# Optimization experiments

Measured on AMD Instinct MI355X. Metric: run time of the kernel, lower is better.

## Reference

```python
import jax, jax.numpy as jnp
import numpy as np

N = 255  # 17 * time_input(15) graph nodes


def spmm(rows, cols, vals, x):
    """Batched sparse (COO) @ dense: x is [B, N, F] -> [B, N, F]."""
    g = x[:, cols, :] * vals[None, :, None]                      # [B, nnz, F]
    out = jax.ops.segment_sum(jnp.swapaxes(g, 0, 1), rows,
                              num_segments=N)                     # [N, B, F]
    return jnp.swapaxes(out, 0, 1)


def setup_inputs() -> dict:
    key = jax.random.key(0)
    ks = jax.random.split(key, 32)
    B, nnz = 256, 2040
    inp = {"H": jax.random.normal(ks[0], (B, N, 2), jnp.float32)}
    for i, nm in enumerate(["sm_s", "sm_t", "sp_s", "sp_t"]):
        inp[nm + "_rows"] = jax.random.randint(ks[1 + 3 * i], (nnz,), 0, N, jnp.int32)
        inp[nm + "_cols"] = jax.random.randint(ks[2 + 3 * i], (nnz,), 0, N, jnp.int32)
        inp[nm + "_vals"] = jax.random.uniform(ks[3 + 3 * i], (nnz,), jnp.float32)
    dims = [(2, 400), (400, 300), (300, 100), (100, 300), (300, 400), (400, 2)]
    wnames = ["W0", "W1", "W2", "Wd0", "Wd1", "Wd2"]
    for j, (di, do) in enumerate(dims):
        inp[wnames[j]] = jax.random.normal(ks[13 + j], (di, do), jnp.float32) / np.sqrt(di).astype(np.float32)
        inp["b" + wnames[j][1:]] = jnp.zeros((do,), jnp.float32)
    return inp


def reference(H, sm_s_rows, sm_s_cols, sm_s_vals,
              sm_t_rows, sm_t_cols, sm_t_vals,
              sp_s_rows, sp_s_cols, sp_s_vals,
              sp_t_rows, sp_t_cols, sp_t_vals,
              W0, b0, W1, b1, W2, b2, Wd0, bd0, Wd1, bd1, Wd2, bd2):
    def layer(x, W, b, r, c, v):
        # Dense projection fused with Laplacian SpMM + ReLU (same math as the
        # per-sample Python loop in the original, batched over B).
        return jax.nn.relu(spmm(r, c, v, x @ W + b))

    # encoder: Laplacian smoothing (enc0, enc1 with s_DADsm; enc2 with t_DADsm)
    H = layer(H, W0, b0, sm_s_rows, sm_s_cols, sm_s_vals)
    H = layer(H, W1, b1, sm_s_rows, sm_s_cols, sm_s_vals)
    H = layer(H, W2, b2, sm_t_rows, sm_t_cols, sm_t_vals)
    # decoder: Laplacian sharpening (dec0 with t_DADsp; dec1, dec2 with s_DADsp)
    H = layer(H, Wd0, bd0, sp_t_rows, sp_t_cols, sp_t_vals)
    H = layer(H, Wd1, bd1, sp_s_rows, sp_s_cols, sp_s_vals)
    H = layer(H, Wd2, bd2, sp_s_rows, sp_s_cols, sp_s_vals)
    return H  # [B, 255, 2]
```

## Files before the change

### kernel.cpp

```cpp
#include <hip/hip_runtime.h>
#include <hip/hip_bf16.h>


#define NN 255
#define YCH 4096

typedef __attribute__((ext_vector_type(8))) short short8;
typedef __attribute__((ext_vector_type(4))) float floatx4;

__device__ __forceinline__ float bf2f(ushort u) {
    union { uint u; float f; } c; c.u = ((uint)u) << 16; return c.f;
}
__device__ __forceinline__ ushort f2bf(float f) {
    union { float f; uint u; } c; c.f = f;
    uint u = c.u + 0x7fff + ((c.u >> 16) & 1);
    return (ushort)(u >> 16);
}
__device__ __forceinline__ short8 u4_frag(uint4 v) {
    union { uint4 u; short8 s; } c; c.u = v; return c.s;
}
__device__ __forceinline__ void gl_lds16(const ushort* g, ushort* l) {
    __builtin_amdgcn_global_load_lds(
        (const __attribute__((address_space(1))) void*)g,
        (__attribute__((address_space(3))) void*)l, 16, 0, 0);
}

__global__ void zero_k(int* p, int n) {
    int i = blockIdx.x * blockDim.x + threadIdx.x;
    if (i < n) p[i] = 0;
}

__global__ void edge_k(const int* __restrict__ r0, const int* __restrict__ c0, const float* __restrict__ v0,
                       const int* __restrict__ r1, const int* __restrict__ c1, const float* __restrict__ v1,
                       const int* __restrict__ r2, const int* __restrict__ c2, const float* __restrict__ v2,
                       const int* __restrict__ r3, const int* __restrict__ c3, const float* __restrict__ v3,
                       float* Sd, float* rs, int nnz) {
    int gi = blockIdx.y;
    int e = blockIdx.x * blockDim.x + threadIdx.x;
    if (e >= nnz) return;
    const int* rr = gi == 0 ? r0 : gi == 1 ? r1 : gi == 2 ? r2 : r3;
    const int* cc = gi == 0 ? c0 : gi == 1 ? c1 : gi == 2 ? c2 : c3;
    const float* vv = gi == 0 ? v0 : gi == 1 ? v1 : gi == 2 ? v2 : v3;
    int r = rr[e], c = cc[e];
    float v = vv[e];
    atomicAdd(&Sd[gi * 65536 + r * 256 + c], v);
    atomicAdd(&rs[gi * 256 + r], v);
}

__device__ __forceinline__ void wpiece(const float* __restrict__ W, ushort* __restrict__ Wt,
                                       int K, int N, int Kpad, int idx) {
    int n = idx / Kpad, k = idx - n * Kpad;
    float v = (n < N && k < K) ? W[(size_t)k * N + n] : 0.f;
    Wt[idx] = f2bf(v);
}

__global__ void conv_k(const float* __restrict__ Sd, ushort* __restrict__ Sb,
                       const float* __restrict__ W1, ushort* __restrict__ Wt1,
                       const float* __restrict__ W2, ushort* __restrict__ Wt2,
                       const float* __restrict__ W3, ushort* __restrict__ Wt3,
                       const float* __restrict__ W4, ushort* __restrict__ Wt4) {
    int idx = blockIdx.x * blockDim.x + threadIdx.x;
    if (idx < 262144) { Sb[idx] = f2bf(Sd[idx]); return; }
    idx -= 262144;
    if (idx < 159744) { wpiece(W1, Wt1, 400, 300, 416, idx); return; }
    idx -= 159744;
    if (idx < 40960)  { wpiece(W2, Wt2, 300, 100, 320, idx); return; }
    idx -= 40960;
    if (idx < 49152)  { wpiece(W3, Wt3, 100, 300, 128, idx); return; }
    idx -= 49152;
    if (idx < 163840) { wpiece(W4, Wt4, 300, 400, 320, idx); }
}

__global__ __launch_bounds__(256) void l0_fused(const float* __restrict__ H,
                                                const float* __restrict__ Sd0,
                                                const float* __restrict__ W0,
                                                const float* __restrict__ b0,
                                                const float* __restrict__ rs0,
                                                ushort* __restrict__ Y) {
    __shared__ float hsh[512];
    __shared__ float ssh[512];
    int b = blockIdx.x, t = threadIdx.x;
    if (t < NN) {
        hsh[t * 2]     = H[((size_t)b * NN + t) * 2];
        hsh[t * 2 + 1] = H[((size_t)b * NN + t) * 2 + 1];
    } else {
        hsh[t * 2] = 0.f; hsh[t * 2 + 1] = 0.f;
    }
    __syncthreads();
    const float4* Sr = (const float4*)(Sd0 + (size_t)t * 256);
    float s0 = 0.f, s1 = 0.f;
    #pragma unroll 8
    for (int c4 = 0; c4 < 64; ++c4) {
        float4 v = Sr[c4];
        const float2* hp = (const float2*)&hsh[c4 * 8];
        float2 h0 = hp[0], h1 = hp[1], h2 = hp[2], h3 = hp[3];
        s0 = fmaf(v.x, h0.x, s0); s1 = fmaf(v.x, h0.y, s1);
        s0 = fmaf(v.y, h1.x, s0); s1 = fmaf(v.y, h1.y, s1);
        s0 = fmaf(v.z, h2.x, s0); s1 = fmaf(v.z, h2.y, s1);
        s0 = fmaf(v.w, h3.x, s0); s1 = fmaf(v.w, h3.y, s1);
    }
    ssh[t * 2] = s0; ssh[t * 2 + 1] = s1;
    __syncthreads();
    uint* out = (uint*)(Y + (((size_t)b) << 8) * 416);
    for (int i = 0; i < 200; ++i) {
        int idx = i * 256 + t;
        int m = idx / 200, n2 = idx - m * 200;
        int n = n2 * 2;
        float x0 = ssh[m * 2], x1 = ssh[m * 2 + 1];
        float rsm = rs0[m];
        float y0 = fmaf(x0, W0[n],     fmaf(x1, W0[400 + n],     rsm * b0[n]));
        float y1 = fmaf(x0, W0[n + 1], fmaf(x1, W0[400 + n + 1], rsm * b0[n + 1]));
        out[(size_t)m * 208 + n2] =
            (uint)f2bf(fmaxf(y0, 0.f)) | ((uint)f2bf(fmaxf(y1, 0.f)) << 16);
    }
}

__global__ __launch_bounds__(512, 4) void fused_layer(const ushort* __restrict__ X,
                                                      const ushort* __restrict__ Wt,
                                                      const ushort* __restrict__ Sg,
                                                      const float* __restrict__ bias,
                                                      ushort* __restrict__ Z,
                                                      int Kpad, int Nfeat, int FsN,
                                                      int nft) {
    __shared__ __align__(16) ushort smem[32768];
    ushort* As0 = smem;
    ushort* As1 = smem + 4096;
    ushort* As2 = smem + 8192;
    ushort* Bs0 = smem + 12288;
    ushort* Bs1 = smem + 20480;
    ushort* Ys  = smem;

    int li = blockIdx.x;
    int x = li & 7, rr = li >> 3;
    int ft = rr % nft, b = (rr / nft) * 8 + x;
    int f0 = ft * 128;

    int t = threadIdx.x;
    int w = t >> 6, lane = t & 63;
    int frow = lane & 15, quad = lane >> 4;
    int rot = ((quad + (frow >> 2)) & 3) * 8;

    const ushort* Xb = X + (((size_t)b) << 8) * (size_t)Kpad;
    const ushort* gB0 = Xb + (size_t)(32 * w +  0 + (lane >> 2)) * Kpad + (lane & 3) * 8;
    const ushort* gB1 = Xb + (size_t)(32 * w + 16 + (lane >> 2)) * Kpad + (lane & 3) * 8;
    const ushort* gA0 = Wt + (size_t)(f0 + 16 * w + (lane >> 2)) * Kpad + (lane & 3) * 8;

    floatx4 acc[2][8];
    #pragma unroll
    for (int i = 0; i < 2; ++i)
        #pragma unroll
        for (int j = 0; j < 8; ++j) acc[i][j] = (floatx4)0.f;

    int nk1 = Kpad >> 5;

    {
        ushort* Bd = Bs0 + w * 1024;
        gl_lds16(gB0, Bd);  gl_lds16(gB1, Bd + 512);
        gl_lds16(gA0, As0 + w * 512);
        ushort* Bd1 = Bs1 + w * 1024;
        gl_lds16(gB0 + 32, Bd1);  gl_lds16(gB1 + 32, Bd1 + 512);
        gl_lds16(gA0 + 32, As1 + w * 512);
    }
    __builtin_amdgcn_sched_barrier(0);
    asm volatile("s_waitcnt vmcnt(3)" ::: "memory");
    __builtin_amdgcn_s_barrier();
    __builtin_amdgcn_sched_barrier(0);

    ushort *a0 = As0, *a1 = As1, *a2 = As2;
    ushort *bc = Bs0, *bn = Bs1;

    for (int ks = 0; ks < nk1; ++ks) {
        const ushort* Ab = a0 + frow * 32 + quad * 8;
        const ushort* Bb = bc + (w * 32 + frow) * 32 + quad * 8;
        short8 xf[2], wf[8];
        #pragma unroll
        for (int i = 0; i < 2; ++i)
            xf[i] = u4_frag(*(const uint4*)(Bb + i * 512));
        #pragma unroll
        for (int j = 0; j < 8; ++j)
            wf[j] = u4_frag(*(const uint4*)(Ab + j * 512));
        asm volatile("s_waitcnt lgkmcnt(0)" ::: "memory");
        __builtin_amdgcn_sched_barrier(0);
        if (ks + 2 < nk1) {
            int off = (ks + 2) * 32;
            ushort* Bd = bc + w * 1024;
            gl_lds16(gB0 + off, Bd);  gl_lds16(gB1 + off, Bd + 512);
            gl_lds16(gA0 + off, a2 + w * 512);
        }
        #pragma unroll
        for (int i = 0; i < 2; ++i)
            #pragma unroll
            for (int j = 0; j < 8; ++j)
                acc[i][j] = __builtin_amdgcn_mfma_f32_16x16x32_bf16(xf[i], wf[j], acc[i][j], 0, 0, 0);
        __builtin_amdgcn_sched_barrier(0);
        if (ks + 2 < nk1)
            asm volatile("s_waitcnt vmcnt(3)" ::: "memory");
        else
            asm volatile("s_waitcnt vmcnt(0)" ::: "memory");
        __builtin_amdgcn_s_barrier();
        __builtin_amdgcn_sched_barrier(0);
        ushort* ta = a0; a0 = a1; a1 = a2; a2 = ta;
        ushort* tb = bc; bc = bn; bn = tb;
    }

    const ushort* Sp = Sg + (size_t)(w * 32 + frow) * 256 + quad * 8;
    uint4 ps[2];
    #pragma unroll
    for (int i = 0; i < 2; ++i) ps[i] = *(const uint4*)(Sp + i * 4096);

    #pragma unroll
    for (int j = 0; j < 8; ++j) {
        int f = j * 16 + frow;
        float bv = (f0 + f < Nfeat) ? bias[f0 + f] : 0.f;
        #pragma unroll
        for (int i = 0; i < 2; ++i) {
            int gc = 2 * i + (quad >> 1);
            int base = w * YCH + f * 32 + (((gc + (frow >> 2)) & 3) * 8) + (quad & 1) * 4;
            uint lo = (uint)f2bf(acc[i][j][0] + bv) | ((uint)f2bf(acc[i][j][1] + bv) << 16);
            uint hi = (uint)f2bf(acc[i][j][2] + bv) | ((uint)f2bf(acc[i][j][3] + bv) << 16);
            *(uint2*)(&Ys[base]) = make_uint2(lo, hi);
        }
    }
    __syncthreads();

    #pragma unroll
    for (int i = 0; i < 2; ++i)
        #pragma unroll
        for (int j = 0; j < 8; ++j) acc[i][j] = (floatx4)0.f;

    for (int ks = 0; ks < 8; ++ks) {
        uint4 pn[2];
        if (ks < 7) {
            #pragma unroll
            for (int i = 0; i < 2; ++i)
                pn[i] = *(const uint4*)(Sp + i * 4096 + (ks + 1) * 32);
        }
        short8 bf[8];
        #pragma unroll
        for (int j = 0; j < 8; ++j)
            bf[j] = u4_frag(*(const uint4*)(&Ys[ks * YCH + (j * 16 + frow) * 32 + rot]));
        #pragma unroll
        for (int i = 0; i < 2; ++i) {
            short8 af = u4_frag(ps[i]);
            #pragma unroll
            for (int j = 0; j < 8; ++j)
                acc[i][j] = __builtin_amdgcn_mfma_f32_16x16x32_bf16(af, bf[j], acc[i][j], 0, 0, 0);
        }
        #pragma unroll
        for (int i = 0; i < 2; ++i) ps[i] = pn[i];
    }

    #pragma unroll
    for (int i = 0; i < 2; ++i)
        #pragma unroll
        for (int r = 0; r < 4; ++r) {
            int rg = w * 32 + i * 16 + quad * 4 + r;
            ushort* Zr = Z + (size_t)((b << 8) + rg) * FsN + f0;
            #pragma unroll
            for (int j = 0; j < 8; ++j)
                if (f0 + j * 16 < FsN)
                    Zr[j * 16 + frow] = f2bf(fmaxf(acc[i][j][r], 0.f));
        }
}

__global__ __launch_bounds__(256) void l5_fused(const ushort* __restrict__ X,
                                                const float* __restrict__ Sd2,
                                                const float* __restrict__ Wd2,
                                                const float* __restrict__ bd2,
                                                float* __restrict__ out) {
    __shared__ float ysh[512];
    int b = blockIdx.x, t = threadIdx.x;
    const uint4* Xr = (const uint4*)(X + ((size_t)((b << 8) + t)) * 448);
    const float4* Wp = (const float4*)Wd2;
    float a0 = bd2[0], a1 = bd2[1];
    for (int i = 0; i < 50; ++i) {
        uint4 p = Xr[i];
        uint pv[4] = {p.x, p.y, p.z, p.w};
        #pragma unroll
        for (int q = 0; q < 4; ++q) {
            float x0 = bf2f((ushort)(pv[q] & 0xffffu));
            float x1 = bf2f((ushort)(pv[q] >> 16));
            float4 w = Wp[i * 4 + q];
            a0 = fmaf(x0, w.x, a0); a1 = fmaf(x0, w.y, a1);
            a0 = fmaf(x1, w.z, a0); a1 = fmaf(x1, w.w, a1);
        }
    }
    ysh[t * 2] = a0; ysh[t * 2 + 1] = a1;
    __syncthreads();
    if (t < NN) {
        const float4* Sr = (const float4*)(Sd2 + (size_t)t * 256);
        float s0 = 0.f, s1 = 0.f;
        #pragma unroll 8
        for (int c4 = 0; c4 < 64; ++c4) {
            float4 v = Sr[c4];
            const float2* yp = (const float2*)&ysh[c4 * 8];
            float2 y0 = yp[0], y1 = yp[1], y2 = yp[2], y3 = yp[3];
            s0 = fmaf(v.x, y0.x, s0); s1 = fmaf(v.x, y0.y, s1);
            s0 = fmaf(v.y, y1.x, s0); s1 = fmaf(v.y, y1.y, s1);
            s0 = fmaf(v.z, y2.x, s0); s1 = fmaf(v.z, y2.y, s1);
            s0 = fmaf(v.w, y3.x, s0); s1 = fmaf(v.w, y3.y, s1);
        }
        out[((size_t)b * NN + t) * 2]     = fmaxf(s0, 0.f);
        out[((size_t)b * NN + t) * 2 + 1] = fmaxf(s1, 0.f);
    }
}

extern "C" void kernel_launch(void* const* d_in, const int* in_sizes, int n_in,
                              void* d_out, int out_size, void* d_ws, size_t ws_size,
                              hipStream_t stream) {
    const float* H = (const float*)d_in[0];
    const int*   g_rows[4] = {(const int*)d_in[1], (const int*)d_in[4], (const int*)d_in[7], (const int*)d_in[10]};
    const int*   g_cols[4] = {(const int*)d_in[2], (const int*)d_in[5], (const int*)d_in[8], (const int*)d_in[11]};
    const float* g_vals[4] = {(const float*)d_in[3], (const float*)d_in[6], (const float*)d_in[9], (const float*)d_in[12]};
    const float* W0  = (const float*)d_in[13]; const float* b0  = (const float*)d_in[14];
    const float* W1  = (const float*)d_in[15]; const float* b1  = (const float*)d_in[16];
    const float* W2  = (const float*)d_in[17]; const float* b2  = (const float*)d_in[18];
    const float* Wd0 = (const float*)d_in[19]; const float* bd0 = (const float*)d_in[20];
    const float* Wd1 = (const float*)d_in[21]; const float* bd1 = (const float*)d_in[22];
    const float* Wd2 = (const float*)d_in[23]; const float* bd2 = (const float*)d_in[24];
    float* out = (float*)d_out;

    const int nnz = in_sizes[1];
    const int B   = in_sizes[0] / (NN * 2);
    const int Mp  = B * 256;

    ushort* bufA = (ushort*)d_ws;
    ushort* bufB = bufA + (size_t)Mp * 448;
    ushort* Wt1 = bufB + (size_t)Mp * 320;
    ushort* Wt2 = Wt1 + 384 * 416;
    ushort* Wt3 = Wt2 + 128 * 320;
    ushort* Wt4 = Wt3 + 384 * 128;
    ushort* Sb  = Wt4 + 512 * 320;
    float*  rs  = (float*)(Sb + 4 * 65536);
    float*  Sd  = rs + 4 * 256;
    const int ZN = 4 * 256 + 4 * 65536;

    zero_k<<<(ZN + 255) / 256, 256, 0, stream>>>((int*)rs, ZN);
    edge_k<<<dim3((nnz + 255) / 256, 4), 256, 0, stream>>>(
        g_rows[0], g_cols[0], g_vals[0], g_rows[1], g_cols[1], g_vals[1],
        g_rows[2], g_cols[2], g_vals[2], g_rows[3], g_cols[3], g_vals[3],
        Sd, rs, nnz);
    conv_k<<<(675840 + 255) / 256, 256, 0, stream>>>(Sd, Sb, W1, Wt1, W2, Wt2, Wd0, Wt3, Wd1, Wt4);

    l0_fused<<<B, 256, 0, stream>>>(H, Sd + 0 * 65536, W0, b0, rs + 0, bufA);

    fused_layer<<<B * 3, 512, 0, stream>>>(bufA, Wt1, Sb + 0 * 65536, b1, bufB, 416, 300, 320, 3);
    fused_layer<<<B * 1, 512, 0, stream>>>(bufB, Wt2, Sb + 1 * 65536, b2, bufA, 320, 100, 128, 1);
    fused_layer<<<B * 3, 512, 0, stream>>>(bufA, Wt3, Sb + 3 * 65536, bd0, bufB, 128, 300, 320, 3);
    fused_layer<<<B * 4, 512, 0, stream>>>(bufB, Wt4, Sb + 2 * 65536, bd1, bufA, 320, 400, 448, 4);

    l5_fused<<<B, 256, 0, stream>>>(bufA, Sd + 2 * 65536, Wd2, bd2, out);
}
```

Before: 315.6 us.

## Retile SpMM stage as 4x4 fragment grid per wave and use packed bf16 converts

The second-stage GEMM (dense Laplacian S times projected Y in LDS) now gives each wave a 64-row by 64-feature block with a 4x4 MFMA grid, instead of 32 rows by 128 features. This is meant to balance reuse of A fragments from global memory against B fragments from LDS, halving the LDS fragment reads per MFMA. Manual bf16 rounding is replaced by the hardware v_cvt_pk_bf16_f32 instruction for the Y store and the Z epilogue. The rounding behaviour of the hardware conversion may differ slightly for NaNs, and waves whose feature block lies beyond FsN now skip the whole epilogue.

```diff
diff --git a/kernel.cpp b/kernel.cpp
--- a/kernel.cpp
+++ b/kernel.cpp
@@ -15,6 +15,11 @@
     union { float f; uint u; } c; c.f = f;
     uint u = c.u + 0x7fff + ((c.u >> 16) & 1);
     return (ushort)(u >> 16);
+}
+__device__ __forceinline__ uint cvt_pk_bf16(float a, float b) {
+    uint r;
+    asm("v_cvt_pk_bf16_f32 %0, %1, %2" : "=v"(r) : "v"(a), "v"(b));
+    return r;
 }
 __device__ __forceinline__ short8 u4_frag(uint4 v) {
     union { uint4 u; short8 s; } c; c.u = v; return c.s;
@@ -203,10 +208,11 @@
         ushort* tb = bc; bc = bn; bn = tb;
     }
 
-    const ushort* Sp = Sg + (size_t)(w * 32 + frow) * 256 + quad * 8;
-    uint4 ps[2];
+    int wr = w & 3, wf = w >> 2;
+    const ushort* Sp = Sg + (size_t)(wr * 64 + frow) * 256 + quad * 8;
+    uint4 ps[4];
     #pragma unroll
-    for (int i = 0; i < 2; ++i) ps[i] = *(const uint4*)(Sp + i * 4096);
+    for (int i = 0; i < 4; ++i) ps[i] = *(const uint4*)(Sp + i * 4096);
 
     #pragma unroll
     for (int j = 0; j < 8; ++j) {
@@ -216,51 +222,57 @@
         for (int i = 0; i < 2; ++i) {
             int gc = 2 * i + (quad >> 1);
             int base = w * YCH + f * 32 + (((gc + (frow >> 2)) & 3) * 8) + (quad & 1) * 4;
-            uint lo = (uint)f2bf(acc[i][j][0] + bv) | ((uint)f2bf(acc[i][j][1] + bv) << 16);
-            uint hi = (uint)f2bf(acc[i][j][2] + bv) | ((uint)f2bf(acc[i][j][3] + bv) << 16);
+            uint lo = cvt_pk_bf16(acc[i][j][0] + bv, acc[i][j][1] + bv);
+            uint hi = cvt_pk_bf16(acc[i][j][2] + bv, acc[i][j][3] + bv);
             *(uint2*)(&Ys[base]) = make_uint2(lo, hi);
         }
     }
     __syncthreads();
 
+    floatx4 acc2[4][4];
     #pragma unroll
-    for (int i = 0; i < 2; ++i)
-        #pragma unroll
-        for (int j = 0; j < 8; ++j) acc[i][j] = (floatx4)0.f;
+    for (int i = 0; i < 4; ++i)
+        #pragma unroll
+        for (int j = 0; j < 4; ++j) acc2[i][j] = (floatx4)0.f;
 
     for (int ks = 0; ks < 8; ++ks) {
-        uint4 pn[2];
+        uint4 pn[4];
         if (ks < 7) {
             #pragma unroll
-            for (int i = 0; i < 2; ++i)
+            for (int i = 0; i < 4; ++i)
                 pn[i] = *(const uint4*)(Sp + i * 4096 + (ks + 1) * 32);
         }
-        short8 bf[8];
-        #pragma unroll
-        for (int j = 0; j < 8; ++j)
-            bf[j] = u4_frag(*(const uint4*)(&Ys[ks * YCH + (j * 16 + frow) * 32 + rot]));
-        #pragma unroll
-        for (int i = 0; i < 2; ++i) {
+        short8 bf[4];
+        #pragma unroll
+        for (int j = 0; j < 4; ++j)
+            bf[j] = u4_frag(*(const uint4*)(&Ys[ks * YCH + (wf * 64 + j * 16 + frow) * 32 + rot]));
+        #pragma unroll
+        for (int i = 0; i < 4; ++i) {
             short8 af = u4_frag(ps[i]);
             #pragma unroll
-            for (int j = 0; j < 8; ++j)
-                acc[i][j] = __builtin_amdgcn_mfma_f32_16x16x32_bf16(af, bf[j], acc[i][j], 0, 0, 0);
-        }
-        #pragma unroll
-        for (int i = 0; i < 2; ++i) ps[i] = pn[i];
-    }
-
-    #pragma unroll
-    for (int i = 0; i < 2; ++i)
-        #pragma unroll
-        for (int r = 0; r < 4; ++r) {
-            int rg = w * 32 + i * 16 + quad * 4 + r;
-            ushort* Zr = Z + (size_t)((b << 8) + rg) * FsN + f0;
+            for (int j = 0; j < 4; ++j)
+                acc2[i][j] = __builtin_amdgcn_mfma_f32_16x16x32_bf16(af, bf[j], acc2[i][j], 0, 0, 0);
+        }
+        #pragma unroll
+        for (int i = 0; i < 4; ++i) ps[i] = pn[i];
+    }
+
+    int fbase = f0 + wf * 64;
+    if (fbase < FsN) {
+        #pragma unroll
+        for (int i = 0; i < 4; ++i)
             #pragma unroll
-            for (int j = 0; j < 8; ++j)
-                if (f0 + j * 16 < FsN)
-                    Zr[j * 16 + frow] = f2bf(fmaxf(acc[i][j][r], 0.f));
-        }
+            for (int r = 0; r < 4; ++r) {
+                int rg = wr * 64 + i * 16 + quad * 4 + r;
+                ushort* Zr = Z + (size_t)((b << 8) + rg) * FsN + fbase;
+                uint u01 = cvt_pk_bf16(fmaxf(acc2[i][0][r], 0.f), fmaxf(acc2[i][1][r], 0.f));
+                uint u23 = cvt_pk_bf16(fmaxf(acc2[i][2][r], 0.f), fmaxf(acc2[i][3][r], 0.f));
+                Zr[frow]      = (ushort)u01;
+                Zr[16 + frow] = (ushort)(u01 >> 16);
+                Zr[32 + frow] = (ushort)u23;
+                Zr[48 + frow] = (ushort)(u23 >> 16);
+            }
+    }
 }
 
 __global__ __launch_bounds__(256) void l5_fused(const ushort* __restrict__ X,
```

New measurement: 346.7 us. 1.1x slower.
